# Performance work log

Measured on AMD Instinct MI355X. Metric: run time of the kernel, lower is better.

The kernel has to match this reference:

```python
import jax, jax.numpy as jnp
import numpy as np

B, N, F_IN, UNITS, E, MAX_VIEW = 4, 10000, 64, 64, 160000, 3
C = F_IN + UNITS  # concat channel dim (num_embedding)


def setup_inputs() -> dict:
    key = jax.random.key(0)
    ks = jax.random.split(key, 8)
    inputs = jax.random.normal(ks[0], (B, N, F_IN), jnp.float32)
    hx = jax.random.normal(ks[1], (B, N, UNITS), jnp.float32)
    sparse_idx = jax.random.randint(ks[2], (2, E), 0, N)          # row0=src, row1=dst
    conv_ker = jax.random.normal(ks[3], (E,), jnp.float32) * 0.1  # per-edge kernel weight
    W_ru = jax.random.normal(ks[4], (MAX_VIEW * C, 2 * UNITS), jnp.float32) * 0.05
    b_ru = jnp.zeros((2 * UNITS,), jnp.float32)
    W_c = jax.random.normal(ks[5], (MAX_VIEW * C, UNITS), jnp.float32) * 0.05
    b_c = jnp.zeros((UNITS,), jnp.float32)
    return dict(inputs=inputs, hx=hx, sparse_idx=sparse_idx, conv_ker=conv_ker,
                W_ru=W_ru, b_ru=b_ru, W_c=W_c, b_c=b_c)


def _graph_conv(x, src, dst, ker, W, b):
    """Multi-view sparse graph conv: [x, A x, A^2 x, ...] concat -> linear.
    x: (B, N, C); edge e aggregates ker[e] * x[:, src[e]] into node dst[e]."""
    views = [x]
    y = x
    for _ in range(MAX_VIEW - 1):
        msg = y[:, src, :] * ker[None, :, None]        # (B, E, C) gather + scale
        y = jnp.zeros_like(x).at[:, dst, :].add(msg)   # (B, N, C) scatter-add
        views.append(y)
    h = jnp.concatenate(views, axis=-1)                # (B, N, MAX_VIEW*C)
    return h @ W + b


def reference(inputs, hx, sparse_idx, conv_ker, W_ru, b_ru, W_c, b_c):
    src, dst = sparse_idx[0], sparse_idx[1]
    # GRU r,u gates from graph conv over concat(inputs, hx)
    x_ru = jnp.concatenate([inputs, hx], axis=-1)                      # (B, N, C)
    ru = jax.nn.sigmoid(_graph_conv(x_ru, src, dst, conv_ker, W_ru, b_ru))
    r, u = jnp.split(ru, 2, axis=-1)                                   # (B, N, UNITS) each
    # candidate state from graph conv over concat(inputs, r*hx)
    x_c = jnp.concatenate([inputs, r * hx], axis=-1)
    c = jnp.tanh(_graph_conv(x_c, src, dst, conv_ker, W_c, b_c))
    return u * hx + (1.0 - u) * c
```

## Files before the change

kernel.cpp:

```cpp
#include <hip/hip_runtime.h>
#include <hip/hip_bf16.h>
#include <math.h>

#define NB 10000
#define BB 4
#define EE 160000
#define MM (NB * BB)
#define SLOTS 64

typedef __attribute__((ext_vector_type(8))) short short8;
typedef __attribute__((ext_vector_type(4))) float floatx4;

struct ViewTab {
  const ushort* base[12];
  int stride[12];
};


__device__ inline unsigned pk(float a, float b) {
  __hip_bfloat16 ha = __float2bfloat16(a), hb = __float2bfloat16(b);
  unsigned short ua = *(unsigned short*)&ha, ub = *(unsigned short*)&hb;
  return (unsigned)ua | ((unsigned)ub << 16);
}

__device__ inline float bf2f(ushort u) {
  unsigned v = (unsigned)u << 16;
  return __uint_as_float(v);
}

__device__ inline void fma8(float* a, uint4 v, float k) {
  a[0] += k * __uint_as_float(v.x << 16);
  a[1] += k * __uint_as_float(v.x & 0xffff0000u);
  a[2] += k * __uint_as_float(v.y << 16);
  a[3] += k * __uint_as_float(v.y & 0xffff0000u);
  a[4] += k * __uint_as_float(v.z << 16);
  a[5] += k * __uint_as_float(v.z & 0xffff0000u);
  a[6] += k * __uint_as_float(v.w << 16);
  a[7] += k * __uint_as_float(v.w & 0xffff0000u);
}


__global__ __launch_bounds__(256) void k_misc(
    const int* __restrict__ src, const int* __restrict__ dst,
    const float* __restrict__ ker, int* __restrict__ cnt,
    uint2* __restrict__ edges,
    const float* __restrict__ in, const float* __restrict__ hx,
    ushort* __restrict__ x,
    const float* __restrict__ Wru, const float* __restrict__ Wc,
    ushort* __restrict__ Wtru, ushort* __restrict__ Wtc) {
  int blk = blockIdx.x;
  if (blk < 625) {
    int e = blk * 256 + threadIdx.x;
    if (e < EE) {
      int n = dst[e];
      int slot = atomicAdd(&cnt[n], 1);
      if (slot < SLOTS)
        edges[(size_t)n * SLOTS + slot] =
            make_uint2((unsigned)src[e], __float_as_uint(ker[e]));
    }
  } else if (blk < 3125) {
    int tid = (blk - 625) * 256 + threadIdx.x;
    int m = tid >> 4;
    int c8 = (tid & 15) << 3;
    const float* sp = (c8 < 64) ? (in + (size_t)m * 64 + c8)
                                : (hx + (size_t)m * 64 + (c8 - 64));
    float4 f0 = *(const float4*)(sp);
    float4 f1 = *(const float4*)(sp + 4);
    uint4 o;
    o.x = pk(f0.x, f0.y); o.y = pk(f0.z, f0.w);
    o.z = pk(f1.x, f1.y); o.w = pk(f1.z, f1.w);
    *(uint4*)(x + (size_t)m * 128 + c8) = o;
  } else {
    int t = (blk - 3125) * 256 + threadIdx.x;
    int nn = t / 384, kk = t % 384;
    __hip_bfloat16 h = __float2bfloat16(Wru[(size_t)kk * 128 + nn]);
    Wtru[t] = *(unsigned short*)&h;
    if (t < 64 * 384) {
      __hip_bfloat16 h2 = __float2bfloat16(Wc[(size_t)kk * 64 + nn]);
      Wtc[t] = *(unsigned short*)&h2;
    }
  }
}


__global__ __launch_bounds__(256) void k_prop128(const ushort* __restrict__ x,
                                                 ushort* __restrict__ y,
                                                 const int* __restrict__ cnt,
                                                 const uint2* __restrict__ edges) {
  int blk = blockIdx.x;
  int b = (blk & 7) >> 1;
  int jb = ((blk >> 3) << 1) | (blk & 1);
  int w = threadIdx.x >> 6;
  int lane = threadIdx.x & 63;
  int n = jb * 4 + w;
  int g = lane >> 4;
  int o8 = (lane & 15) << 3;
  const ushort* xb = x + (size_t)b * NB * 128;
  const uint2* ebase = edges + (size_t)n * SLOTS;
  int deg = min(cnt[n], SLOTS);
  float acc[8];
#pragma unroll
  for (int j = 0; j < 8; ++j) acc[j] = 0.f;
  int i = g;
  for (; i + 12 < deg; i += 16) {
    uint2 e0 = ebase[i], e1 = ebase[i + 4], e2 = ebase[i + 8], e3 = ebase[i + 12];
    uint4 v0 = *(const uint4*)(xb + (size_t)e0.x * 128 + o8);
    uint4 v1 = *(const uint4*)(xb + (size_t)e1.x * 128 + o8);
    uint4 v2 = *(const uint4*)(xb + (size_t)e2.x * 128 + o8);
    uint4 v3 = *(const uint4*)(xb + (size_t)e3.x * 128 + o8);
    fma8(acc, v0, __uint_as_float(e0.y));
    fma8(acc, v1, __uint_as_float(e1.y));
    fma8(acc, v2, __uint_as_float(e2.y));
    fma8(acc, v3, __uint_as_float(e3.y));
  }
  for (; i < deg; i += 4) {
    uint2 e0 = ebase[i];
    uint4 v0 = *(const uint4*)(xb + (size_t)e0.x * 128 + o8);
    fma8(acc, v0, __uint_as_float(e0.y));
  }
#pragma unroll
  for (int j = 0; j < 8; ++j) {
    acc[j] += __shfl_xor(acc[j], 16);
    acc[j] += __shfl_xor(acc[j], 32);
  }
  if (g == 0) {
    uint4 o;
    o.x = pk(acc[0], acc[1]); o.y = pk(acc[2], acc[3]);
    o.z = pk(acc[4], acc[5]); o.w = pk(acc[6], acc[7]);
    *(uint4*)(y + (size_t)b * NB * 128 + (size_t)n * 128 + o8) = o;
  }
}

__global__ __launch_bounds__(256) void k_prop64(const ushort* __restrict__ x,
                                                ushort* __restrict__ y,
                                                const int* __restrict__ cnt,
                                                const uint2* __restrict__ edges) {
  int blk = blockIdx.x;
  int b = (blk & 7) >> 1;
  int jb = ((blk >> 3) << 1) | (blk & 1);
  int w = threadIdx.x >> 6;
  int lane = threadIdx.x & 63;
  int n = jb * 4 + w;
  int g = lane >> 3;
  int o8 = (lane & 7) << 3;
  const ushort* xb = x + (size_t)b * NB * 64;
  const uint2* ebase = edges + (size_t)n * SLOTS;
  int deg = min(cnt[n], SLOTS);
  float acc[8];
#pragma unroll
  for (int j = 0; j < 8; ++j) acc[j] = 0.f;
  int i = g;
  for (; i + 8 < deg; i += 16) {
    uint2 e0 = ebase[i], e1 = ebase[i + 8];
    uint4 v0 = *(const uint4*)(xb + (size_t)e0.x * 64 + o8);
    uint4 v1 = *(const uint4*)(xb + (size_t)e1.x * 64 + o8);
    fma8(acc, v0, __uint_as_float(e0.y));
    fma8(acc, v1, __uint_as_float(e1.y));
  }
  for (; i < deg; i += 8) {
    uint2 e0 = ebase[i];
    uint4 v0 = *(const uint4*)(xb + (size_t)e0.x * 64 + o8);
    fma8(acc, v0, __uint_as_float(e0.y));
  }
#pragma unroll
  for (int j = 0; j < 8; ++j) {
    acc[j] += __shfl_xor(acc[j], 8);
    acc[j] += __shfl_xor(acc[j], 16);
    acc[j] += __shfl_xor(acc[j], 32);
  }
  if (g == 0) {
    uint4 o;
    o.x = pk(acc[0], acc[1]); o.y = pk(acc[2], acc[3]);
    o.z = pk(acc[4], acc[5]); o.w = pk(acc[6], acc[7]);
    *(uint4*)(y + (size_t)b * NB * 64 + (size_t)n * 64 + o8) = o;
  }
}


template <bool FINAL>
__global__ __launch_bounds__(256) void k_gemm_mfma(
    ViewTab V, const ushort* __restrict__ Wt, const float* __restrict__ bias,
    ushort* __restrict__ rh0, ushort* __restrict__ u,
    const ushort* __restrict__ uu, const float* __restrict__ hx,
    float* __restrict__ out) {
  const int tid = threadIdx.x;
  const int lane = tid & 63;
  const int w = tid >> 6;
  const int rt = FINAL ? blockIdx.x : (blockIdx.x >> 1);
  const int colbase = FINAL ? 0 : ((blockIdx.x & 1) * 64);
  const int m0 = rt * 64 + w * 16;
  const int lr = lane & 15;
  const int quad = lane >> 4;
  const int koff = quad * 8;

  short8 a[12];
#pragma unroll
  for (int kt = 0; kt < 12; ++kt) {
    a[kt] = *(const short8*)(V.base[kt] + (size_t)(m0 + lr) * V.stride[kt] + koff);
  }

  floatx4 acc[4];
#pragma unroll
  for (int nt = 0; nt < 4; ++nt) acc[nt] = {0.f, 0.f, 0.f, 0.f};

  const ushort* wrow = Wt + (size_t)(colbase + lr) * 384 + koff;
  short8 bcur[4];
#pragma unroll
  for (int nt = 0; nt < 4; ++nt) bcur[nt] = *(const short8*)(wrow + nt * (16 * 384));

#pragma unroll
  for (int kt = 0; kt < 12; ++kt) {
    short8 bnext[4];
    if (kt < 11) {
#pragma unroll
      for (int nt = 0; nt < 4; ++nt)
        bnext[nt] = *(const short8*)(wrow + nt * (16 * 384) + (kt + 1) * 32);
    }
#pragma unroll
    for (int nt = 0; nt < 4; ++nt)
      acc[nt] = __builtin_amdgcn_mfma_f32_16x16x32_bf16(a[kt], bcur[nt], acc[nt], 0, 0, 0);
    if (kt < 11) {
#pragma unroll
      for (int nt = 0; nt < 4; ++nt) bcur[nt] = bnext[nt];
    }
  }

#pragma unroll
  for (int nt = 0; nt < 4; ++nt) {
    int col = colbase + nt * 16 + lr;
    float bv = bias[col];
#pragma unroll
    for (int i = 0; i < 4; ++i) {
      int m = m0 + quad * 4 + i;
      float val = acc[nt][i] + bv;
      if (!FINAL) {
        float s = 1.f / (1.f + expf(-val));
        if (col < 64) {
          float r = s * hx[(size_t)m * 64 + col];
          __hip_bfloat16 hb = __float2bfloat16(r);
          rh0[(size_t)m * 64 + col] = *(unsigned short*)&hb;
        } else {
          __hip_bfloat16 hb = __float2bfloat16(s);
          u[(size_t)m * 64 + (col - 64)] = *(unsigned short*)&hb;
        }
      } else {
        float uv = bf2f(uu[(size_t)m * 64 + col]);
        float h = hx[(size_t)m * 64 + col];
        float c = tanhf(val);
        out[(size_t)m * 64 + col] = uv * h + (1.f - uv) * c;
      }
    }
  }
}


extern "C" void kernel_launch(void* const* d_in, const int* in_sizes, int n_in,
                              void* d_out, int out_size, void* d_ws, size_t ws_size,
                              hipStream_t stream) {
  const float* d_inputs = (const float*)d_in[0];
  const float* d_hx     = (const float*)d_in[1];
  const int*   d_sidx   = (const int*)d_in[2];
  const float* d_ker    = (const float*)d_in[3];
  const float* d_Wru    = (const float*)d_in[4];
  const float* d_bru    = (const float*)d_in[5];
  const float* d_Wc     = (const float*)d_in[6];
  const float* d_bc     = (const float*)d_in[7];
  float* out = (float*)d_out;
  const int* src = d_sidx;
  const int* dst = d_sidx + EE;

  ushort* x    = (ushort*)d_ws;
  ushort* y1   = x + (size_t)MM * 128;
  ushort* y2   = y1 + (size_t)MM * 128;
  ushort* rh0  = y2 + (size_t)MM * 128;
  ushort* rh1  = rh0 + (size_t)MM * 64;
  ushort* rh2  = rh1 + (size_t)MM * 64;
  ushort* u    = rh2 + (size_t)MM * 64;
  ushort* Wtru = u + (size_t)MM * 64;
  ushort* Wtc  = Wtru + 128 * 384;
  uint2*  edges = (uint2*)(Wtc + 64 * 384);
  int*    cnt  = (int*)(edges + (size_t)NB * SLOTS);

  hipMemsetAsync(cnt, 0, NB * sizeof(int), stream);
  k_misc<<<3317, 256, 0, stream>>>(src, dst, d_ker, cnt, edges,
                                   d_inputs, d_hx, x, d_Wru, d_Wc, Wtru, Wtc);

  k_prop128<<<10000, 256, 0, stream>>>(x, y1, cnt, edges);
  k_prop128<<<10000, 256, 0, stream>>>(y1, y2, cnt, edges);
  ViewTab V1;
  for (int t = 0; t < 12; ++t) {
    const ushort* ten = (t < 4) ? x : (t < 8) ? y1 : y2;
    V1.base[t] = ten + (t & 3) * 32;
    V1.stride[t] = 128;
  }
  k_gemm_mfma<false><<<1250, 256, 0, stream>>>(V1, Wtru, d_bru, rh0, u,
                                               nullptr, d_hx, nullptr);

  k_prop64<<<10000, 256, 0, stream>>>(rh0, rh1, cnt, edges);
  k_prop64<<<10000, 256, 0, stream>>>(rh1, rh2, cnt, edges);
  ViewTab V2;
  {
    const ushort* c1[3] = {x, y1, y2};
    const ushort* c2[3] = {rh0, rh1, rh2};
    for (int v = 0; v < 3; ++v) {
      V2.base[v * 4 + 0] = c1[v];      V2.stride[v * 4 + 0] = 128;
      V2.base[v * 4 + 1] = c1[v] + 32; V2.stride[v * 4 + 1] = 128;
      V2.base[v * 4 + 2] = c2[v];      V2.stride[v * 4 + 2] = 64;
      V2.base[v * 4 + 3] = c2[v] + 32; V2.stride[v * 4 + 3] = 64;
    }
  }
  k_gemm_mfma<true><<<625, 256, 0, stream>>>(V2, Wtc, d_bc, nullptr, nullptr,
                                             u, d_hx, out);
}
```

Baseline: 233.8 us.

## Precompute candidate-gate input contribution in first GEMM, split second GEMM

The first GEMM kernel now also computes the candidate gate's contribution from the input channels of each view (which equal the inputs part of x, y1, y2), reusing the already-loaded A fragments, and stores it as a bf16 partial. The second GEMM then only multiplies the r*hx propagated views (K=192 instead of 384) and adds the stored partial. The change also drops the column-split grid and the B prefetch. It is meant to avoid reloading x/y1/y2 in the final GEMM, at the cost of an extra bf16 partial buffer written and read, one more rounding step, and higher register pressure in k_gemm1.

```diff
diff --git a/kernel.cpp b/kernel.cpp
--- a/kernel.cpp
+++ b/kernel.cpp
@@ -11,11 +11,6 @@
 typedef __attribute__((ext_vector_type(8))) short short8;
 typedef __attribute__((ext_vector_type(4))) float floatx4;
 
-struct ViewTab {
-  const ushort* base[12];
-  int stride[12];
-};
-
 
 __device__ inline unsigned pk(float a, float b) {
   __hip_bfloat16 ha = __float2bfloat16(a), hb = __float2bfloat16(b);
@@ -26,6 +21,11 @@
 __device__ inline float bf2f(ushort u) {
   unsigned v = (unsigned)u << 16;
   return __uint_as_float(v);
+}
+
+__device__ inline ushort f2bf(float f) {
+  __hip_bfloat16 h = __float2bfloat16(f);
+  return *(unsigned short*)&h;
 }
 
 __device__ inline void fma8(float* a, uint4 v, float k) {
@@ -47,7 +47,8 @@
     const float* __restrict__ in, const float* __restrict__ hx,
     ushort* __restrict__ x,
     const float* __restrict__ Wru, const float* __restrict__ Wc,
-    ushort* __restrict__ Wtru, ushort* __restrict__ Wtc) {
+    ushort* __restrict__ Wtru, ushort* __restrict__ Wtcin,
+    ushort* __restrict__ Wtc2) {
   int blk = blockIdx.x;
   if (blk < 625) {
     int e = blk * 256 + threadIdx.x;
@@ -73,11 +74,12 @@
   } else {
     int t = (blk - 3125) * 256 + threadIdx.x;
     int nn = t / 384, kk = t % 384;
-    __hip_bfloat16 h = __float2bfloat16(Wru[(size_t)kk * 128 + nn]);
-    Wtru[t] = *(unsigned short*)&h;
-    if (t < 64 * 384) {
-      __hip_bfloat16 h2 = __float2bfloat16(Wc[(size_t)kk * 64 + nn]);
-      Wtc[t] = *(unsigned short*)&h2;
+    Wtru[t] = f2bf(Wru[(size_t)kk * 128 + nn]);
+    if (t < 64 * 192) {
+      int n2 = t / 192, k = t % 192;
+      int v = k >> 6, kv = k & 63;
+      Wtcin[t] = f2bf(Wc[(size_t)(v * 128 + kv) * 64 + n2]);
+      Wtc2[t]  = f2bf(Wc[(size_t)(v * 128 + 64 + kv) * 64 + n2]);
     }
   }
 }
@@ -177,78 +179,143 @@
 }
 
 
-template <bool FINAL>
-__global__ __launch_bounds__(256) void k_gemm_mfma(
-    ViewTab V, const ushort* __restrict__ Wt, const float* __restrict__ bias,
-    ushort* __restrict__ rh0, ushort* __restrict__ u,
+__global__ __launch_bounds__(256) void k_gemm1(
+    const ushort* __restrict__ x, const ushort* __restrict__ y1,
+    const ushort* __restrict__ y2, const ushort* __restrict__ Wtru,
+    const ushort* __restrict__ Wtcin, const float* __restrict__ bias,
+    const float* __restrict__ hx, ushort* __restrict__ rh0,
+    ushort* __restrict__ u, ushort* __restrict__ cp) {
+  const int tid = threadIdx.x;
+  const int lane = tid & 63;
+  const int w = tid >> 6;
+  const int m0 = blockIdx.x * 64 + w * 16;
+  const int lr = lane & 15;
+  const int quad = lane >> 4;
+  const int koff = quad * 8;
+
+  const ushort* vb[3] = {x, y1, y2};
+  short8 a[12];
+#pragma unroll
+  for (int v = 0; v < 3; ++v)
+#pragma unroll
+    for (int h = 0; h < 4; ++h)
+      a[v * 4 + h] = *(const short8*)(vb[v] + (size_t)(m0 + lr) * 128 + h * 32 + koff);
+  float hxv[16];
+#pragma unroll
+  for (int nt = 0; nt < 4; ++nt)
+#pragma unroll
+    for (int i = 0; i < 4; ++i)
+      hxv[nt * 4 + i] = hx[(size_t)(m0 + quad * 4 + i) * 64 + nt * 16 + lr];
+
+  floatx4 aru[8], ac[4];
+#pragma unroll
+  for (int nt = 0; nt < 8; ++nt) aru[nt] = {0.f, 0.f, 0.f, 0.f};
+#pragma unroll
+  for (int nt = 0; nt < 4; ++nt) ac[nt] = {0.f, 0.f, 0.f, 0.f};
+
+#pragma unroll
+  for (int kt = 0; kt < 12; ++kt) {
+    const int v = kt >> 2, h = kt & 3;
+    const int kg = kt * 32 + koff;
+#pragma unroll
+    for (int nt = 0; nt < 8; ++nt) {
+      short8 b = *(const short8*)(Wtru + (size_t)(nt * 16 + lr) * 384 + kg);
+      aru[nt] = __builtin_amdgcn_mfma_f32_16x16x32_bf16(a[kt], b, aru[nt], 0, 0, 0);
+    }
+    if (h < 2) {
+      const int kgc = v * 64 + h * 32 + koff;
+#pragma unroll
+      for (int nt = 0; nt < 4; ++nt) {
+        short8 b = *(const short8*)(Wtcin + (size_t)(nt * 16 + lr) * 192 + kgc);
+        ac[nt] = __builtin_amdgcn_mfma_f32_16x16x32_bf16(a[kt], b, ac[nt], 0, 0, 0);
+      }
+    }
+  }
+
+#pragma unroll
+  for (int nt = 0; nt < 8; ++nt) {
+    int col = nt * 16 + lr;
+    float bv = bias[col];
+#pragma unroll
+    for (int i = 0; i < 4; ++i) {
+      int m = m0 + quad * 4 + i;
+      float s = 1.f / (1.f + expf(-(aru[nt][i] + bv)));
+      if (nt < 4) {
+        rh0[(size_t)m * 64 + col] = f2bf(s * hxv[nt * 4 + i]);
+      } else {
+        u[(size_t)m * 64 + (col - 64)] = f2bf(s);
+      }
+    }
+  }
+#pragma unroll
+  for (int nt = 0; nt < 4; ++nt) {
+    int col = nt * 16 + lr;
+#pragma unroll
+    for (int i = 0; i < 4; ++i) {
+      int m = m0 + quad * 4 + i;
+      cp[(size_t)m * 64 + col] = f2bf(ac[nt][i]);
+    }
+  }
+}
+
+
+__global__ __launch_bounds__(256) void k_gemm2(
+    const ushort* __restrict__ rh0, const ushort* __restrict__ rh1,
+    const ushort* __restrict__ rh2, const ushort* __restrict__ Wtc2,
+    const float* __restrict__ bias, const ushort* __restrict__ cp,
     const ushort* __restrict__ uu, const float* __restrict__ hx,
     float* __restrict__ out) {
   const int tid = threadIdx.x;
   const int lane = tid & 63;
   const int w = tid >> 6;
-  const int rt = FINAL ? blockIdx.x : (blockIdx.x >> 1);
-  const int colbase = FINAL ? 0 : ((blockIdx.x & 1) * 64);
-  const int m0 = rt * 64 + w * 16;
+  const int m0 = blockIdx.x * 64 + w * 16;
   const int lr = lane & 15;
   const int quad = lane >> 4;
   const int koff = quad * 8;
 
-  short8 a[12];
-#pragma unroll
-  for (int kt = 0; kt < 12; ++kt) {
-    a[kt] = *(const short8*)(V.base[kt] + (size_t)(m0 + lr) * V.stride[kt] + koff);
-  }
+  const ushort* vb[3] = {rh0, rh1, rh2};
+  short8 a[6];
+#pragma unroll
+  for (int v = 0; v < 3; ++v)
+#pragma unroll
+    for (int h = 0; h < 2; ++h)
+      a[v * 2 + h] = *(const short8*)(vb[v] + (size_t)(m0 + lr) * 64 + h * 32 + koff);
+
+  float cpv[16], uv[16], hxv[16];
+#pragma unroll
+  for (int nt = 0; nt < 4; ++nt)
+#pragma unroll
+    for (int i = 0; i < 4; ++i) {
+      size_t idx = (size_t)(m0 + quad * 4 + i) * 64 + nt * 16 + lr;
+      cpv[nt * 4 + i] = bf2f(cp[idx]);
+      uv[nt * 4 + i] = bf2f(uu[idx]);
+      hxv[nt * 4 + i] = hx[idx];
+    }
 
   floatx4 acc[4];
 #pragma unroll
   for (int nt = 0; nt < 4; ++nt) acc[nt] = {0.f, 0.f, 0.f, 0.f};
 
-  const ushort* wrow = Wt + (size_t)(colbase + lr) * 384 + koff;
-  short8 bcur[4];
-#pragma unroll
-  for (int nt = 0; nt < 4; ++nt) bcur[nt] = *(const short8*)(wrow + nt * (16 * 384));
-
-#pragma unroll
-  for (int kt = 0; kt < 12; ++kt) {
-    short8 bnext[4];
-    if (kt < 11) {
-#pragma unroll
-      for (int nt = 0; nt < 4; ++nt)
-        bnext[nt] = *(const short8*)(wrow + nt * (16 * 384) + (kt + 1) * 32);
-    }
-#pragma unroll
-    for (int nt = 0; nt < 4; ++nt)
-      acc[nt] = __builtin_amdgcn_mfma_f32_16x16x32_bf16(a[kt], bcur[nt], acc[nt], 0, 0, 0);
-    if (kt < 11) {
-#pragma unroll
-      for (int nt = 0; nt < 4; ++nt) bcur[nt] = bnext[nt];
+#pragma unroll
+  for (int kt = 0; kt < 6; ++kt) {
+    const int kg = kt * 32 + koff;
+#pragma unroll
+    for (int nt = 0; nt < 4; ++nt) {
+      short8 b = *(const short8*)(Wtc2 + (size_t)(nt * 16 + lr) * 192 + kg);
+      acc[nt] = __builtin_amdgcn_mfma_f32_16x16x32_bf16(a[kt], b, acc[nt], 0, 0, 0);
     }
   }
 
 #pragma unroll
   for (int nt = 0; nt < 4; ++nt) {
-    int col = colbase + nt * 16 + lr;
+    int col = nt * 16 + lr;
     float bv = bias[col];
 #pragma unroll
     for (int i = 0; i < 4; ++i) {
       int m = m0 + quad * 4 + i;
-      float val = acc[nt][i] + bv;
-      if (!FINAL) {
-        float s = 1.f / (1.f + expf(-val));
-        if (col < 64) {
-          float r = s * hx[(size_t)m * 64 + col];
-          __hip_bfloat16 hb = __float2bfloat16(r);
-          rh0[(size_t)m * 64 + col] = *(unsigned short*)&hb;
-        } else {
-          __hip_bfloat16 hb = __float2bfloat16(s);
-          u[(size_t)m * 64 + (col - 64)] = *(unsigned short*)&hb;
-        }
-      } else {
-        float uv = bf2f(uu[(size_t)m * 64 + col]);
-        float h = hx[(size_t)m * 64 + col];
-        float c = tanhf(val);
-        out[(size_t)m * 64 + col] = uv * h + (1.f - uv) * c;
-      }
+      int j = nt * 4 + i;
+      float c = tanhf(acc[nt][i] + cpv[j] + bv);
+      out[(size_t)m * 64 + col] = uv[j] * hxv[j] + (1.f - uv[j]) * c;
     }
   }
 }
@@ -269,46 +336,31 @@
   const int* src = d_sidx;
   const int* dst = d_sidx + EE;
 
-  ushort* x    = (ushort*)d_ws;
-  ushort* y1   = x + (size_t)MM * 128;
-  ushort* y2   = y1 + (size_t)MM * 128;
-  ushort* rh0  = y2 + (size_t)MM * 128;
-  ushort* rh1  = rh0 + (size_t)MM * 64;
-  ushort* rh2  = rh1 + (size_t)MM * 64;
-  ushort* u    = rh2 + (size_t)MM * 64;
-  ushort* Wtru = u + (size_t)MM * 64;
-  ushort* Wtc  = Wtru + 128 * 384;
-  uint2*  edges = (uint2*)(Wtc + 64 * 384);
-  int*    cnt  = (int*)(edges + (size_t)NB * SLOTS);
+  ushort* x     = (ushort*)d_ws;
+  ushort* y1    = x + (size_t)MM * 128;
+  ushort* y2    = y1 + (size_t)MM * 128;
+  ushort* rh0   = y2 + (size_t)MM * 128;
+  ushort* rh1   = rh0 + (size_t)MM * 64;
+  ushort* rh2   = rh1 + (size_t)MM * 64;
+  ushort* u     = rh2 + (size_t)MM * 64;
+  ushort* cp    = u + (size_t)MM * 64;
+  ushort* Wtru  = cp + (size_t)MM * 64;
+  ushort* Wtcin = Wtru + 128 * 384;
+  ushort* Wtc2  = Wtcin + 64 * 192;
+  uint2*  edges = (uint2*)(Wtc2 + 64 * 192);
+  int*    cnt   = (int*)(edges + (size_t)NB * SLOTS);
 
   hipMemsetAsync(cnt, 0, NB * sizeof(int), stream);
   k_misc<<<3317, 256, 0, stream>>>(src, dst, d_ker, cnt, edges,
-                                   d_inputs, d_hx, x, d_Wru, d_Wc, Wtru, Wtc);
+                                   d_inputs, d_hx, x, d_Wru, d_Wc,
+                                   Wtru, Wtcin, Wtc2);
 
   k_prop128<<<10000, 256, 0, stream>>>(x, y1, cnt, edges);
   k_prop128<<<10000, 256, 0, stream>>>(y1, y2, cnt, edges);
-  ViewTab V1;
-  for (int t = 0; t < 12; ++t) {
-    const ushort* ten = (t < 4) ? x : (t < 8) ? y1 : y2;
-    V1.base[t] = ten + (t & 3) * 32;
-    V1.stride[t] = 128;
-  }
-  k_gemm_mfma<false><<<1250, 256, 0, stream>>>(V1, Wtru, d_bru, rh0, u,
-                                               nullptr, d_hx, nullptr);
+  k_gemm1<<<625, 256, 0, stream>>>(x, y1, y2, Wtru, Wtcin, d_bru, d_hx,
+                                   rh0, u, cp);
 
   k_prop64<<<10000, 256, 0, stream>>>(rh0, rh1, cnt, edges);
   k_prop64<<<10000, 256, 0, stream>>>(rh1, rh2, cnt, edges);
-  ViewTab V2;
-  {
-    const ushort* c1[3] = {x, y1, y2};
-    const ushort* c2[3] = {rh0, rh1, rh2};
-    for (int v = 0; v < 3; ++v) {
-      V2.base[v * 4 + 0] = c1[v];      V2.stride[v * 4 + 0] = 128;
-      V2.base[v * 4 + 1] = c1[v] + 32; V2.stride[v * 4 + 1] = 128;
-      V2.base[v * 4 + 2] = c2[v];      V2.stride[v * 4 + 2] = 64;
-      V2.base[v * 4 + 3] = c2[v] + 32; V2.stride[v * 4 + 3] = 64;
-    }
-  }
-  k_gemm_mfma<true><<<625, 256, 0, stream>>>(V2, Wtc, d_bc, nullptr, nullptr,
-                                             u, d_hx, out);
-}
+  k_gemm2<<<625, 256, 0, stream>>>(rh0, rh1, rh2, Wtc2, d_bc, cp, u, d_hx, out);
+}
```

New measurement: 234.7 us. No clear change (+0.4%).
